# Optimization experiments

Hardware: AMD Instinct MI355X
Metric: run time of the kernel (lower is better)

The kernel has to match this reference:

```python
import jax, jax.numpy as jnp
import numpy as np
from jax import lax

B, D, T = 8, 128, 4096
Q, C = 30, 1024


def setup_inputs() -> dict:
    key = jax.random.key(0)
    k1, k2 = jax.random.split(key)
    x = jax.random.normal(k1, (B, D, T), dtype=jnp.float32)
    codebooks = jax.random.normal(k2, (Q, C, D), dtype=jnp.float32)
    return {"x": x, "codebooks": codebooks}


def _vq_step(residual, cb):
    # residual: [B, T, D], cb: [C, D]
    # argmin over squared euclidean distance; ||r||^2 term is constant per row
    scores = -2.0 * jnp.einsum("btd,cd->btc", residual, cb) + jnp.sum(cb * cb, axis=-1)  # [B,T,C]
    idx = jnp.argmin(scores, axis=-1)          # [B,T]
    quant = cb[idx]                            # [B,T,D] gather
    # commitment loss: mse(quantize.detach(), residual)
    loss = jnp.mean((lax.stop_gradient(quant) - residual) ** 2)
    # straight-through estimator
    quant_st = residual + lax.stop_gradient(quant - residual)
    new_residual = residual - lax.stop_gradient(quant)
    return new_residual, (quant_st, loss)


def reference(x, codebooks):
    # x: [B, D, T] -> [B, T, D]
    xt = jnp.transpose(x, (0, 2, 1))
    _, (quants, losses) = lax.scan(_vq_step, xt, codebooks)  # quants: [Q,B,T,D]
    quantized = jnp.sum(quants, axis=0)                      # [B,T,D]
    quantized = jnp.transpose(quantized, (0, 2, 1))          # [B,D,T]
    commit_loss = jnp.sum(losses)
    return quantized, commit_loss
```

## Files before the change

kernel.cpp:

```cpp
#include <hip/hip_runtime.h>
#include <stdint.h>

#define B_ 8
#define D_ 128
#define T_ 4096
#define Q_ 30
#define C_ 1024

typedef __attribute__((ext_vector_type(8))) short short8;
typedef __attribute__((ext_vector_type(4))) float float4_;

__device__ __align__(16) short g_split[(size_t)Q_*16*16384];

__device__ __forceinline__ unsigned short f2bf(float f){
  unsigned u = __builtin_bit_cast(unsigned, f);
  u += 0x7fffu + ((u>>16)&1u);
  return (unsigned short)(u>>16);
}
__device__ __forceinline__ float bf2f(unsigned short h){
  unsigned u = ((unsigned)h)<<16;
  return __builtin_bit_cast(float, u);
}

typedef __attribute__((address_space(3))) void lds_void;
typedef __attribute__((address_space(1))) const void gbl_void;
__device__ __forceinline__ void gld16(const void* g, void* l){
  __builtin_amdgcn_global_load_lds((gbl_void*)g, (lds_void*)l, 16, 0, 0);
}

__global__ void rvq_prep(const float* __restrict__ cb, float* __restrict__ sumsq){
  int g    = blockIdx.x*128 + (threadIdx.x>>1);
  int half = threadIdx.x & 1;
  const float* src = cb + (size_t)g*D_ + half*64;
  double s = 0.0;
#pragma unroll
  for (int i=0;i<64;i+=4){
    float4_ f = *(const float4_*)(src+i);
    s += (double)f.x*f.x + (double)f.y*f.y + (double)f.z*f.z + (double)f.w*f.w;
  }
  s += __shfl_xor(s, 1);
  if (!half) sumsq[g] = (float)s;
}

__global__ void rvq_split(const float* __restrict__ cb){
  const int bI   = blockIdx.x;
  const int tid  = threadIdx.x;
  const int crel = tid>>2, part = tid&3;
  const int swz  = crel & 15;
  const float* src = cb + ((size_t)(bI*64 + crel))*128 + part*32;
  short* dstH = g_split + ((size_t)bI<<14) + (crel<<7);
#pragma unroll
  for (int i=0;i<32;i+=8){
    float4_ f0 = *(const float4_*)(src+i);
    float4_ f1 = *(const float4_*)(src+i+4);
    float ff[8] = {f0.x,f0.y,f0.z,f0.w,f1.x,f1.y,f1.z,f1.w};
    short8 vh, vl;
#pragma unroll
    for (int j=0;j<8;++j){
      unsigned short hb = f2bf(ff[j]);
      vh[j] = (short)hb;
      vl[j] = (short)f2bf(ff[j] - bf2f(hb));
    }
    const int kgs = ((part<<2) + (i>>3)) ^ swz;
    *(short8*)&dstH[kgs<<3]          = vh;
    *(short8*)&dstH[8192 + (kgs<<3)] = vl;
  }
}

__global__ __launch_bounds__(256,1) void rvq_main(
    const float* __restrict__ x, const float* __restrict__ cb,
    const float* __restrict__ sumsq, double* __restrict__ lossAcc,
    float* __restrict__ out)
{
  __shared__ short sB[2*16384];
  __shared__ float sCcQ[1024];
  __shared__ int   sIdx[2][128];

  const int tid  = threadIdx.x;
  const int wv   = tid>>6;
  const int ln   = tid&63;
  const int col  = ln&15;
  const int quad = ln>>4;
  const int blk  = blockIdx.x;
  const int b    = blk>>5;
  const int t0   = ((blk&31)<<7) + (wv<<5);

  double rmast[2][4][8];
#pragma unroll
  for (int rt=0;rt<2;++rt){
    const int t = t0 + rt*16 + col;
#pragma unroll
    for (int kc=0;kc<4;++kc)
#pragma unroll
      for (int j=0;j<8;++j){
        const int d = kc*32 + quad*8 + j;
        rmast[rt][kc][j] = (double)x[((size_t)b*D_ + d)*T_ + t];
      }
  }

  short8 ah[2][4], al[2][4];
  auto makeAB = [&](){
#pragma unroll
    for (int rt=0;rt<2;++rt)
#pragma unroll
      for (int kc=0;kc<4;++kc){
        short8 h, l;
#pragma unroll
        for (int j=0;j<8;++j){
          float f = (float)rmast[rt][kc][j];
          unsigned short hb = f2bf(f);
          h[j] = (short)hb;
          l[j] = (short)f2bf(f - bf2f(hb));
        }
        ah[rt][kc] = h; al[rt][kc] = l;
      }
  };
  makeAB();

  auto stage = [&](int gqn){
    const char* gsrc = (const char*)g_split + ((size_t)gqn<<15) + (wv<<13) + (ln<<4);
    char* ldst = (char*)sB + ((gqn&1)<<15) + (wv<<13);
#pragma unroll
    for (int it=0; it<8; ++it)
      gld16(gsrc + it*1024, ldst + it*1024);
  };

  for (int i=tid; i<1024; i+=256) sCcQ[i] = sumsq[i];
  stage(0);
  __syncthreads();

  double lossd = 0.0;

  for (int q=0;q<Q_;++q){
    const float* cbq = cb + (size_t)q*C_*D_;

    float m1[2][4], m2[2][4]; int i1[2][4], i2[2][4];
#pragma unroll
    for (int rt=0;rt<2;++rt)
#pragma unroll
      for (int rg=0;rg<4;++rg){
        m1[rt][rg]=3.0e38f; i1[rt][rg]=0;
        m2[rt][rg]=3.0e38f; i2[rt][rg]=0;
      }

    for (int ch=0; ch<16; ++ch){
      const int gq  = q*16 + ch;
      const int nxt = (gq+1 < Q_*16) ? gq+1 : 0;
      stage(nxt);
      asm volatile("s_waitcnt vmcnt(8)" ::: "memory");
      asm volatile("s_barrier" ::: "memory");
      const int bufS = (gq&1)<<14;

#pragma unroll
      for (int itc=0; itc<2; ++itc){
        float4_ acc[2][2];
#pragma unroll
        for (int a=0;a<2;++a)
#pragma unroll
          for (int c=0;c<2;++c) acc[a][c] = (float4_){0.f,0.f,0.f,0.f};
#pragma unroll
        for (int kc=0;kc<4;++kc){
          short8 bh[2], bl[2];
#pragma unroll
          for (int ct=0;ct<2;++ct){
            const int n   = itc*32 + ct*16 + col;
            const int kgs = ((kc<<2) + quad) ^ col;
            bh[ct] = *(const short8*)&sB[bufS + (n<<7) + (kgs<<3)];
            bl[ct] = *(const short8*)&sB[bufS + 8192 + (n<<7) + (kgs<<3)];
          }
#pragma unroll
          for (int rt=0;rt<2;++rt)
#pragma unroll
            for (int ct=0;ct<2;++ct){
              acc[rt][ct] = __builtin_amdgcn_mfma_f32_16x16x32_bf16(ah[rt][kc], bh[ct], acc[rt][ct], 0,0,0);
              acc[rt][ct] = __builtin_amdgcn_mfma_f32_16x16x32_bf16(ah[rt][kc], bl[ct], acc[rt][ct], 0,0,0);
              acc[rt][ct] = __builtin_amdgcn_mfma_f32_16x16x32_bf16(al[rt][kc], bh[ct], acc[rt][ct], 0,0,0);
            }
        }
        const int itg = ch*2 + itc;
#pragma unroll
        for (int ct=0;ct<2;++ct){
          const float cc = sCcQ[(ch<<6) + itc*32 + ct*16 + col];
          const int cid  = itg*2 + ct;
#pragma unroll
          for (int rt=0;rt<2;++rt)
#pragma unroll
            for (int rg=0;rg<4;++rg){
              float s = fmaf(-2.0f, acc[rt][ct][rg], cc);
              if (s < m1[rt][rg]) {
                m2[rt][rg]=m1[rt][rg]; i2[rt][rg]=i1[rt][rg];
                m1[rt][rg]=s;          i1[rt][rg]=cid;
              } else if (s < m2[rt][rg]) {
                m2[rt][rg]=s;          i2[rt][rg]=cid;
              }
            }
        }
      }
      if (ch != 15)
        asm volatile("s_barrier" ::: "memory");
    }

    float a1[2][4], a2[2][4]; int j1[2][4], j2[2][4];
#pragma unroll
    for (int rt=0;rt<2;++rt)
#pragma unroll
      for (int rg=0;rg<4;++rg){
        a1[rt][rg]=m1[rt][rg]; j1[rt][rg]=(i1[rt][rg]<<4)+col;
        a2[rt][rg]=m2[rt][rg]; j2[rt][rg]=(i2[rt][rg]<<4)+col;
      }
#pragma unroll
    for (int mk=1; mk<16; mk<<=1){
#pragma unroll
      for (int rt=0;rt<2;++rt)
#pragma unroll
        for (int rg=0;rg<4;++rg){
          float b1 = __shfl_xor(a1[rt][rg], mk);
          float b2 = __shfl_xor(a2[rt][rg], mk);
          int   k1 = __shfl_xor(j1[rt][rg], mk);
          int   k2 = __shfl_xor(j2[rt][rg], mk);
          float A1=a1[rt][rg], A2=a2[rt][rg]; int J1=j1[rt][rg], J2=j2[rt][rg];
          bool sw  = (b1 < A1) || (b1 == A1 && k1 < J1);
          float w1 = sw ? b1 : A1; int u1 = sw ? k1 : J1;
          float l1 = sw ? A1 : b1; int v1 = sw ? J1 : k1;
          float o2 = sw ? b2 : A2; int ov = sw ? k2 : J2;
          bool t2  = (o2 < l1) || (o2 == l1 && ov < v1);
          a1[rt][rg]=w1; j1[rt][rg]=u1;
          a2[rt][rg]= t2 ? o2 : l1; j2[rt][rg]= t2 ? ov : v1;
        }
    }
    if (col==0){
#pragma unroll
      for (int rt=0;rt<2;++rt)
#pragma unroll
        for (int rg=0;rg<4;++rg){
          const int m = rt*16 + quad*4 + rg;
          sIdx[0][(wv<<5)+m] = j1[rt][rg];
          sIdx[1][(wv<<5)+m] = j2[rt][rg];
        }
    }
    __syncthreads();

#pragma unroll
    for (int rt=0;rt<2;++rt){
      const int m   = rt*16 + col;
      const int jj1 = sIdx[0][(wv<<5)+m];
      const int jj2 = sIdx[1][(wv<<5)+m];
      const float* p1 = cbq + ((size_t)jj1<<7) + (quad<<3);
      const float* p2 = cbq + ((size_t)jj2<<7) + (quad<<3);
      float c1[4][8], c2[4][8];
#pragma unroll
      for (int kc=0;kc<4;++kc){
        float4_ q10 = *(const float4_*)(p1 + kc*32);
        float4_ q11 = *(const float4_*)(p1 + kc*32 + 4);
        float4_ q20 = *(const float4_*)(p2 + kc*32);
        float4_ q21 = *(const float4_*)(p2 + kc*32 + 4);
        c1[kc][0]=q10.x; c1[kc][1]=q10.y; c1[kc][2]=q10.z; c1[kc][3]=q10.w;
        c1[kc][4]=q11.x; c1[kc][5]=q11.y; c1[kc][6]=q11.z; c1[kc][7]=q11.w;
        c2[kc][0]=q20.x; c2[kc][1]=q20.y; c2[kc][2]=q20.z; c2[kc][3]=q20.w;
        c2[kc][4]=q21.x; c2[kc][5]=q21.y; c2[kc][6]=q21.z; c2[kc][7]=q21.w;
      }
      double s1=0.0, s2=0.0;
#pragma unroll
      for (int kc=0;kc<4;++kc)
#pragma unroll
        for (int j=0;j<8;++j){
          double rd  = rmast[rt][kc][j];
          double cd1 = (double)c1[kc][j];
          double cd2 = (double)c2[kc][j];
          s1 += cd1*(cd1 - 2.0*rd);
          s2 += cd2*(cd2 - 2.0*rd);
        }
      s1 += __shfl_xor(s1, 16); s1 += __shfl_xor(s1, 32);
      s2 += __shfl_xor(s2, 16); s2 += __shfl_xor(s2, 32);
      const bool take2 = (s2 < s1) || (s2 == s1 && jj2 < jj1);
#pragma unroll
      for (int kc=0;kc<4;++kc)
#pragma unroll
        for (int j=0;j<8;++j){
          double cw = (double)(take2 ? c2[kc][j] : c1[kc][j]);
          double rn = rmast[rt][kc][j] - cw;
          rmast[rt][kc][j] = rn;
          lossd += rn*rn;
        }
    }
    makeAB();
    if (q+1 < Q_){
      for (int i=tid; i<1024; i+=256) sCcQ[i] = sumsq[(q+1)*1024 + i];
    }
    __syncthreads();
  }

#pragma unroll
  for (int rt=0;rt<2;++rt){
    const int t = t0 + rt*16 + col;
#pragma unroll
    for (int kc=0;kc<4;++kc)
#pragma unroll
      for (int j=0;j<8;++j){
        const int d = kc*32 + quad*8 + j;
        const size_t o = ((size_t)b*D_ + d)*T_ + t;
        out[o] = (float)((double)x[o] - rmast[rt][kc][j]);
      }
  }
#pragma unroll
  for (int mk=1; mk<64; mk<<=1) lossd += __shfl_xor(lossd, mk);
  if (ln==0) atomicAdd(lossAcc, lossd);
}

__global__ void rvq_fin(const double* __restrict__ lossAcc, float* __restrict__ out){
  out[(size_t)B_*D_*T_] = (float)(*lossAcc * (1.0/((double)B_*(double)D_*(double)T_)));
}

extern "C" void kernel_launch(void* const* d_in, const int* in_sizes, int n_in,
                              void* d_out, int out_size, void* d_ws, size_t ws_size,
                              hipStream_t stream) {
  const float* x  = (const float*)d_in[0];
  const float* cb = (const float*)d_in[1];
  float* out      = (float*)d_out;
  double* lossAcc = (double*)d_ws;
  float*  sumsq   = (float*)((char*)d_ws + 256);

  hipMemsetAsync(d_ws, 0, 256, stream);
  rvq_prep <<<Q_*C_/128, 256, 0, stream>>>(cb, sumsq);
  rvq_split<<<Q_*16,     256, 0, stream>>>(cb);
  rvq_main <<<(B_*T_)/128, 256, 0, stream>>>(x, cb, sumsq, lossAcc, out);
  rvq_fin  <<<1, 1, 0, stream>>>(lossAcc, out);
}
```

Baseline: 1.749 ms.

## Split codebook search across two wave halves per row group with LDS merge

Doubles the block to 512 threads: each group of four row-waves is duplicated, and each half scans 512 of the 1024 codewords, staging its own chunk into a doubled LDS buffer. Per-half top-2 candidates go through shared memory and are merged before the exact double-precision rescoring. Only half 0 writes output and loss. This adds waves per CU to hide MFMA and LDS latency, but duplicates the residual registers and rescoring work in both halves and doubles LDS use. The launch bound also changes to 512 threads with 2 blocks per CU.

```diff
diff --git a/kernel.cpp b/kernel.cpp
--- a/kernel.cpp
+++ b/kernel.cpp
@@ -67,23 +67,26 @@
   }
 }
 
-__global__ __launch_bounds__(256,1) void rvq_main(
+__global__ __launch_bounds__(512,2) void rvq_main(
     const float* __restrict__ x, const float* __restrict__ cb,
     const float* __restrict__ sumsq, double* __restrict__ lossAcc,
     float* __restrict__ out)
 {
-  __shared__ short sB[2*16384];
+  __shared__ short sB[2*32768];
   __shared__ float sCcQ[1024];
-  __shared__ int   sIdx[2][128];
+  __shared__ float sMa[4][2][32][2];
+  __shared__ int   sMj[4][2][32][2];
 
   const int tid  = threadIdx.x;
   const int wv   = tid>>6;
   const int ln   = tid&63;
   const int col  = ln&15;
   const int quad = ln>>4;
+  const int hw   = wv>>2;
+  const int rgrp = wv&3;
   const int blk  = blockIdx.x;
   const int b    = blk>>5;
-  const int t0   = ((blk&31)<<7) + (wv<<5);
+  const int t0   = ((blk&31)<<7) + (rgrp<<5);
 
   double rmast[2][4][8];
 #pragma unroll
@@ -117,15 +120,17 @@
   };
   makeAB();
 
-  auto stage = [&](int gqn){
-    const char* gsrc = (const char*)g_split + ((size_t)gqn<<15) + (wv<<13) + (ln<<4);
-    char* ldst = (char*)sB + ((gqn&1)<<15) + (wv<<13);
+  auto stage = [&](int gstep){
+    const int qq = gstep>>3, cc = gstep&7;
+    const int chunk = qq*16 + hw*8 + cc;
+    const char* gsrc = (const char*)g_split + ((size_t)chunk<<15) + (rgrp<<13) + (ln<<4);
+    char* ldst = (char*)sB + ((gstep&1)<<16) + (hw<<15) + (rgrp<<13);
 #pragma unroll
     for (int it=0; it<8; ++it)
       gld16(gsrc + it*1024, ldst + it*1024);
   };
 
-  for (int i=tid; i<1024; i+=256) sCcQ[i] = sumsq[i];
+  for (int i=tid; i<1024; i+=512) sCcQ[i] = sumsq[i];
   stage(0);
   __syncthreads();
 
@@ -143,13 +148,13 @@
         m2[rt][rg]=3.0e38f; i2[rt][rg]=0;
       }
 
-    for (int ch=0; ch<16; ++ch){
-      const int gq  = q*16 + ch;
-      const int nxt = (gq+1 < Q_*16) ? gq+1 : 0;
+    for (int ch=0; ch<8; ++ch){
+      const int gstep = q*8 + ch;
+      const int nxt   = (gstep+1 < Q_*8) ? gstep+1 : 0;
       stage(nxt);
       asm volatile("s_waitcnt vmcnt(8)" ::: "memory");
       asm volatile("s_barrier" ::: "memory");
-      const int bufS = (gq&1)<<14;
+      const int bufS = ((gstep&1)<<15) + (hw<<14);
 
 #pragma unroll
       for (int itc=0; itc<2; ++itc){
@@ -177,11 +182,10 @@
               acc[rt][ct] = __builtin_amdgcn_mfma_f32_16x16x32_bf16(al[rt][kc], bh[ct], acc[rt][ct], 0,0,0);
             }
         }
-        const int itg = ch*2 + itc;
 #pragma unroll
         for (int ct=0;ct<2;++ct){
-          const float cc = sCcQ[(ch<<6) + itc*32 + ct*16 + col];
-          const int cid  = itg*2 + ct;
+          const float cc = sCcQ[(hw<<9) + (ch<<6) + itc*32 + ct*16 + col];
+          const int cid  = ch*4 + itc*2 + ct;
 #pragma unroll
           for (int rt=0;rt<2;++rt)
 #pragma unroll
@@ -196,7 +200,7 @@
             }
         }
       }
-      if (ch != 15)
+      if (ch != 7)
         asm volatile("s_barrier" ::: "memory");
     }
 
@@ -205,8 +209,8 @@
     for (int rt=0;rt<2;++rt)
 #pragma unroll
       for (int rg=0;rg<4;++rg){
-        a1[rt][rg]=m1[rt][rg]; j1[rt][rg]=(i1[rt][rg]<<4)+col;
-        a2[rt][rg]=m2[rt][rg]; j2[rt][rg]=(i2[rt][rg]<<4)+col;
+        a1[rt][rg]=m1[rt][rg]; j1[rt][rg]=(hw<<9)+(i1[rt][rg]<<4)+col;
+        a2[rt][rg]=m2[rt][rg]; j2[rt][rg]=(hw<<9)+(i2[rt][rg]<<4)+col;
       }
 #pragma unroll
     for (int mk=1; mk<16; mk<<=1){
@@ -234,17 +238,27 @@
 #pragma unroll
         for (int rg=0;rg<4;++rg){
           const int m = rt*16 + quad*4 + rg;
-          sIdx[0][(wv<<5)+m] = j1[rt][rg];
-          sIdx[1][(wv<<5)+m] = j2[rt][rg];
+          sMa[rgrp][hw][m][0] = a1[rt][rg];  sMj[rgrp][hw][m][0] = j1[rt][rg];
+          sMa[rgrp][hw][m][1] = a2[rt][rg];  sMj[rgrp][hw][m][1] = j2[rt][rg];
         }
     }
     __syncthreads();
 
 #pragma unroll
     for (int rt=0;rt<2;++rt){
-      const int m   = rt*16 + col;
-      const int jj1 = sIdx[0][(wv<<5)+m];
-      const int jj2 = sIdx[1][(wv<<5)+m];
+      const int m = rt*16 + col;
+      float x1 = sMa[rgrp][0][m][0], x2 = sMa[rgrp][0][m][1];
+      int  xj1 = sMj[rgrp][0][m][0], xj2 = sMj[rgrp][0][m][1];
+      float y1 = sMa[rgrp][1][m][0], y2 = sMa[rgrp][1][m][1];
+      int  yj1 = sMj[rgrp][1][m][0], yj2 = sMj[rgrp][1][m][1];
+      bool sw  = (y1 < x1) || (y1 == x1 && yj1 < xj1);
+      float w1 = sw ? y1 : x1;  int u1 = sw ? yj1 : xj1;
+      float l1 = sw ? x1 : y1;  int v1 = sw ? xj1 : yj1;
+      float o2 = sw ? y2 : x2;  int ov = sw ? yj2 : xj2;
+      bool t2  = (o2 < l1) || (o2 == l1 && ov < v1);
+      const int jj1 = u1;
+      const int jj2 = t2 ? ov : v1;
+
       const float* p1 = cbq + ((size_t)jj1<<7) + (quad<<3);
       const float* p2 = cbq + ((size_t)jj2<<7) + (quad<<3);
       float c1[4][8], c2[4][8];
@@ -285,26 +299,28 @@
     }
     makeAB();
     if (q+1 < Q_){
-      for (int i=tid; i<1024; i+=256) sCcQ[i] = sumsq[(q+1)*1024 + i];
+      for (int i=tid; i<1024; i+=512) sCcQ[i] = sumsq[(q+1)*1024 + i];
     }
     __syncthreads();
   }
 
-#pragma unroll
-  for (int rt=0;rt<2;++rt){
-    const int t = t0 + rt*16 + col;
-#pragma unroll
-    for (int kc=0;kc<4;++kc)
-#pragma unroll
-      for (int j=0;j<8;++j){
-        const int d = kc*32 + quad*8 + j;
-        const size_t o = ((size_t)b*D_ + d)*T_ + t;
-        out[o] = (float)((double)x[o] - rmast[rt][kc][j]);
-      }
-  }
-#pragma unroll
-  for (int mk=1; mk<64; mk<<=1) lossd += __shfl_xor(lossd, mk);
-  if (ln==0) atomicAdd(lossAcc, lossd);
+  if (hw == 0){
+#pragma unroll
+    for (int rt=0;rt<2;++rt){
+      const int t = t0 + rt*16 + col;
+#pragma unroll
+      for (int kc=0;kc<4;++kc)
+#pragma unroll
+        for (int j=0;j<8;++j){
+          const int d = kc*32 + quad*8 + j;
+          const size_t o = ((size_t)b*D_ + d)*T_ + t;
+          out[o] = (float)((double)x[o] - rmast[rt][kc][j]);
+        }
+    }
+#pragma unroll
+    for (int mk=1; mk<64; mk<<=1) lossd += __shfl_xor(lossd, mk);
+    if (ln==0) atomicAdd(lossAcc, lossd);
+  }
 }
 
 __global__ void rvq_fin(const double* __restrict__ lossAcc, float* __restrict__ out){
@@ -323,6 +339,6 @@
   hipMemsetAsync(d_ws, 0, 256, stream);
   rvq_prep <<<Q_*C_/128, 256, 0, stream>>>(cb, sumsq);
   rvq_split<<<Q_*16,     256, 0, stream>>>(cb);
-  rvq_main <<<(B_*T_)/128, 256, 0, stream>>>(x, cb, sumsq, lossAcc, out);
+  rvq_main <<<(B_*T_)/128, 512, 0, stream>>>(x, cb, sumsq, lossAcc, out);
   rvq_fin  <<<1, 1, 0, stream>>>(lossAcc, out);
 }
```

Result: no change. 1.754 ms (+0.3%).

## Split the D reduction across two wave groups per block with LDS partial-sum exchange

Applied to the files above, without the earlier changes.

Doubles the block to 512 threads. Each pair of waves now splits the 128-dim K reduction in half, with the upper half writing partial MFMA accumulators to LDS and the lower half adding them before the argmin. The rescoring and residual update are likewise split, with partial distances exchanged through shared memory. The goal is twice as many waves per CU to hide latency and fewer registers per wave, at the cost of extra LDS traffic and barriers, plus an argmin that only half the waves perform.

```diff
diff --git a/kernel.cpp b/kernel.cpp
--- a/kernel.cpp
+++ b/kernel.cpp
@@ -67,43 +67,47 @@
   }
 }
 
-__global__ __launch_bounds__(256,1) void rvq_main(
+__global__ __launch_bounds__(512,1) void rvq_main(
     const float* __restrict__ x, const float* __restrict__ cb,
     const float* __restrict__ sumsq, double* __restrict__ lossAcc,
     float* __restrict__ out)
 {
-  __shared__ short sB[2*16384];
-  __shared__ float sCcQ[1024];
-  __shared__ int   sIdx[2][128];
+  __shared__ short  sB[2*16384];
+  __shared__ float  sP[8192];
+  __shared__ float  sCcQ[1024];
+  __shared__ int    sIdx[2][128];
+  __shared__ double sS[2][4][2][2][16];
 
   const int tid  = threadIdx.x;
   const int wv   = tid>>6;
   const int ln   = tid&63;
   const int col  = ln&15;
   const int quad = ln>>4;
+  const int dh   = wv>>2;
+  const int rgrp = wv&3;
   const int blk  = blockIdx.x;
   const int b    = blk>>5;
-  const int t0   = ((blk&31)<<7) + (wv<<5);
-
-  double rmast[2][4][8];
+  const int t0   = ((blk&31)<<7) + (rgrp<<5);
+
+  double rmast[2][2][8];
 #pragma unroll
   for (int rt=0;rt<2;++rt){
     const int t = t0 + rt*16 + col;
 #pragma unroll
-    for (int kc=0;kc<4;++kc)
+    for (int kc=0;kc<2;++kc)
 #pragma unroll
       for (int j=0;j<8;++j){
-        const int d = kc*32 + quad*8 + j;
+        const int d = dh*64 + kc*32 + quad*8 + j;
         rmast[rt][kc][j] = (double)x[((size_t)b*D_ + d)*T_ + t];
       }
   }
 
-  short8 ah[2][4], al[2][4];
+  short8 ah[2][2], al[2][2];
   auto makeAB = [&](){
 #pragma unroll
     for (int rt=0;rt<2;++rt)
 #pragma unroll
-      for (int kc=0;kc<4;++kc){
+      for (int kc=0;kc<2;++kc){
         short8 h, l;
 #pragma unroll
         for (int j=0;j<8;++j){
@@ -117,15 +121,15 @@
   };
   makeAB();
 
-  auto stage = [&](int gqn){
-    const char* gsrc = (const char*)g_split + ((size_t)gqn<<15) + (wv<<13) + (ln<<4);
-    char* ldst = (char*)sB + ((gqn&1)<<15) + (wv<<13);
-#pragma unroll
-    for (int it=0; it<8; ++it)
+  auto stage = [&](int c){
+    const char* gsrc = (const char*)g_split + ((size_t)c<<15) + (wv<<12) + (ln<<4);
+    char* ldst = (char*)sB + ((c&1)<<15) + (wv<<12) + (ln<<4);
+#pragma unroll
+    for (int it=0; it<4; ++it)
       gld16(gsrc + it*1024, ldst + it*1024);
   };
 
-  for (int i=tid; i<1024; i+=256) sCcQ[i] = sumsq[i];
+  for (int i=tid; i<1024; i+=512) sCcQ[i] = sumsq[i];
   stage(0);
   __syncthreads();
 
@@ -135,157 +139,191 @@
     const float* cbq = cb + (size_t)q*C_*D_;
 
     float m1[2][4], m2[2][4]; int i1[2][4], i2[2][4];
-#pragma unroll
-    for (int rt=0;rt<2;++rt)
-#pragma unroll
-      for (int rg=0;rg<4;++rg){
-        m1[rt][rg]=3.0e38f; i1[rt][rg]=0;
-        m2[rt][rg]=3.0e38f; i2[rt][rg]=0;
-      }
+    if (dh==0){
+#pragma unroll
+      for (int rt=0;rt<2;++rt)
+#pragma unroll
+        for (int rg=0;rg<4;++rg){
+          m1[rt][rg]=3.0e38f; i1[rt][rg]=0;
+          m2[rt][rg]=3.0e38f; i2[rt][rg]=0;
+        }
+    }
 
     for (int ch=0; ch<16; ++ch){
-      const int gq  = q*16 + ch;
-      const int nxt = (gq+1 < Q_*16) ? gq+1 : 0;
+      const int c   = q*16 + ch;
+      const int nxt = (c+1 < Q_*16) ? c+1 : 0;
       stage(nxt);
-      asm volatile("s_waitcnt vmcnt(8)" ::: "memory");
+      asm volatile("s_waitcnt vmcnt(4)" ::: "memory");
       asm volatile("s_barrier" ::: "memory");
-      const int bufS = (gq&1)<<14;
-
+      const int slot = (c&1)<<14;
+
+      float4_ accT[2][2][2];
 #pragma unroll
       for (int itc=0; itc<2; ++itc){
-        float4_ acc[2][2];
-#pragma unroll
-        for (int a=0;a<2;++a)
-#pragma unroll
-          for (int c=0;c<2;++c) acc[a][c] = (float4_){0.f,0.f,0.f,0.f};
-#pragma unroll
-        for (int kc=0;kc<4;++kc){
+#pragma unroll
+        for (int rt=0;rt<2;++rt)
+#pragma unroll
+          for (int ct=0;ct<2;++ct) accT[itc][rt][ct] = (float4_){0.f,0.f,0.f,0.f};
+#pragma unroll
+        for (int kc=0;kc<2;++kc){
+          const int kgs = ((dh<<3) + (kc<<2) + quad) ^ col;
           short8 bh[2], bl[2];
 #pragma unroll
           for (int ct=0;ct<2;++ct){
-            const int n   = itc*32 + ct*16 + col;
-            const int kgs = ((kc<<2) + quad) ^ col;
-            bh[ct] = *(const short8*)&sB[bufS + (n<<7) + (kgs<<3)];
-            bl[ct] = *(const short8*)&sB[bufS + 8192 + (n<<7) + (kgs<<3)];
+            const int n = itc*32 + ct*16 + col;
+            bh[ct] = *(const short8*)&sB[slot + (n<<7) + (kgs<<3)];
+            bl[ct] = *(const short8*)&sB[slot + 8192 + (n<<7) + (kgs<<3)];
           }
 #pragma unroll
           for (int rt=0;rt<2;++rt)
 #pragma unroll
             for (int ct=0;ct<2;++ct){
-              acc[rt][ct] = __builtin_amdgcn_mfma_f32_16x16x32_bf16(ah[rt][kc], bh[ct], acc[rt][ct], 0,0,0);
-              acc[rt][ct] = __builtin_amdgcn_mfma_f32_16x16x32_bf16(ah[rt][kc], bl[ct], acc[rt][ct], 0,0,0);
-              acc[rt][ct] = __builtin_amdgcn_mfma_f32_16x16x32_bf16(al[rt][kc], bh[ct], acc[rt][ct], 0,0,0);
+              accT[itc][rt][ct] = __builtin_amdgcn_mfma_f32_16x16x32_bf16(ah[rt][kc], bh[ct], accT[itc][rt][ct], 0,0,0);
+              accT[itc][rt][ct] = __builtin_amdgcn_mfma_f32_16x16x32_bf16(ah[rt][kc], bl[ct], accT[itc][rt][ct], 0,0,0);
+              accT[itc][rt][ct] = __builtin_amdgcn_mfma_f32_16x16x32_bf16(al[rt][kc], bh[ct], accT[itc][rt][ct], 0,0,0);
             }
         }
-        const int itg = ch*2 + itc;
-#pragma unroll
-        for (int ct=0;ct<2;++ct){
-          const float cc = sCcQ[(ch<<6) + itc*32 + ct*16 + col];
-          const int cid  = itg*2 + ct;
+        if (dh==1){
 #pragma unroll
           for (int rt=0;rt<2;++rt)
 #pragma unroll
-            for (int rg=0;rg<4;++rg){
-              float s = fmaf(-2.0f, acc[rt][ct][rg], cc);
-              if (s < m1[rt][rg]) {
-                m2[rt][rg]=m1[rt][rg]; i2[rt][rg]=i1[rt][rg];
-                m1[rt][rg]=s;          i1[rt][rg]=cid;
-              } else if (s < m2[rt][rg]) {
-                m2[rt][rg]=s;          i2[rt][rg]=cid;
+            for (int ct=0;ct<2;++ct){
+              const int idx4 = ((((itc*2+rt)*2+ct)*4 + rgrp)*64 + ln)*4;
+              *(float4_*)&sP[idx4] = accT[itc][rt][ct];
+            }
+        }
+      }
+      asm volatile("s_barrier" ::: "memory");
+
+      if (dh==0){
+#pragma unroll
+        for (int itc=0; itc<2; ++itc)
+#pragma unroll
+          for (int ct=0;ct<2;++ct){
+            const float cc = sCcQ[(ch<<6) + itc*32 + ct*16 + col];
+            const int cid  = ch*4 + itc*2 + ct;
+#pragma unroll
+            for (int rt=0;rt<2;++rt){
+              const int idx4 = ((((itc*2+rt)*2+ct)*4 + rgrp)*64 + ln)*4;
+              float4_ p = *(const float4_*)&sP[idx4];
+#pragma unroll
+              for (int rg=0;rg<4;++rg){
+                float tot = accT[itc][rt][ct][rg] + p[rg];
+                float s = fmaf(-2.0f, tot, cc);
+                if (s < m1[rt][rg]) {
+                  m2[rt][rg]=m1[rt][rg]; i2[rt][rg]=i1[rt][rg];
+                  m1[rt][rg]=s;          i1[rt][rg]=cid;
+                } else if (s < m2[rt][rg]) {
+                  m2[rt][rg]=s;          i2[rt][rg]=cid;
+                }
               }
             }
-        }
-      }
-      if (ch != 15)
-        asm volatile("s_barrier" ::: "memory");
-    }
-
-    float a1[2][4], a2[2][4]; int j1[2][4], j2[2][4];
-#pragma unroll
-    for (int rt=0;rt<2;++rt)
-#pragma unroll
-      for (int rg=0;rg<4;++rg){
-        a1[rt][rg]=m1[rt][rg]; j1[rt][rg]=(i1[rt][rg]<<4)+col;
-        a2[rt][rg]=m2[rt][rg]; j2[rt][rg]=(i2[rt][rg]<<4)+col;
-      }
-#pragma unroll
-    for (int mk=1; mk<16; mk<<=1){
+          }
+      }
+    }
+
+    if (dh==0){
+      float a1[2][4], a2[2][4]; int j1[2][4], j2[2][4];
 #pragma unroll
       for (int rt=0;rt<2;++rt)
 #pragma unroll
         for (int rg=0;rg<4;++rg){
-          float b1 = __shfl_xor(a1[rt][rg], mk);
-          float b2 = __shfl_xor(a2[rt][rg], mk);
-          int   k1 = __shfl_xor(j1[rt][rg], mk);
-          int   k2 = __shfl_xor(j2[rt][rg], mk);
-          float A1=a1[rt][rg], A2=a2[rt][rg]; int J1=j1[rt][rg], J2=j2[rt][rg];
-          bool sw  = (b1 < A1) || (b1 == A1 && k1 < J1);
-          float w1 = sw ? b1 : A1; int u1 = sw ? k1 : J1;
-          float l1 = sw ? A1 : b1; int v1 = sw ? J1 : k1;
-          float o2 = sw ? b2 : A2; int ov = sw ? k2 : J2;
-          bool t2  = (o2 < l1) || (o2 == l1 && ov < v1);
-          a1[rt][rg]=w1; j1[rt][rg]=u1;
-          a2[rt][rg]= t2 ? o2 : l1; j2[rt][rg]= t2 ? ov : v1;
-        }
-    }
-    if (col==0){
-#pragma unroll
-      for (int rt=0;rt<2;++rt)
-#pragma unroll
-        for (int rg=0;rg<4;++rg){
-          const int m = rt*16 + quad*4 + rg;
-          sIdx[0][(wv<<5)+m] = j1[rt][rg];
-          sIdx[1][(wv<<5)+m] = j2[rt][rg];
-        }
+          a1[rt][rg]=m1[rt][rg]; j1[rt][rg]=(i1[rt][rg]<<4)+col;
+          a2[rt][rg]=m2[rt][rg]; j2[rt][rg]=(i2[rt][rg]<<4)+col;
+        }
+#pragma unroll
+      for (int mk=1; mk<16; mk<<=1){
+#pragma unroll
+        for (int rt=0;rt<2;++rt)
+#pragma unroll
+          for (int rg=0;rg<4;++rg){
+            float b1 = __shfl_xor(a1[rt][rg], mk);
+            float b2 = __shfl_xor(a2[rt][rg], mk);
+            int   k1 = __shfl_xor(j1[rt][rg], mk);
+            int   k2 = __shfl_xor(j2[rt][rg], mk);
+            float A1=a1[rt][rg], A2=a2[rt][rg]; int J1=j1[rt][rg], J2=j2[rt][rg];
+            bool sw  = (b1 < A1) || (b1 == A1 && k1 < J1);
+            float w1 = sw ? b1 : A1; int u1 = sw ? k1 : J1;
+            float l1 = sw ? A1 : b1; int v1 = sw ? J1 : k1;
+            float o2 = sw ? b2 : A2; int ov = sw ? k2 : J2;
+            bool t2  = (o2 < l1) || (o2 == l1 && ov < v1);
+            a1[rt][rg]=w1; j1[rt][rg]=u1;
+            a2[rt][rg]= t2 ? o2 : l1; j2[rt][rg]= t2 ? ov : v1;
+          }
+      }
+      if (col==0){
+#pragma unroll
+        for (int rt=0;rt<2;++rt)
+#pragma unroll
+          for (int rg=0;rg<4;++rg){
+            const int m = rt*16 + quad*4 + rg;
+            sIdx[0][(rgrp<<5)+m] = j1[rt][rg];
+            sIdx[1][(rgrp<<5)+m] = j2[rt][rg];
+          }
+      }
     }
     __syncthreads();
 
+    int jjA[2][2];
 #pragma unroll
     for (int rt=0;rt<2;++rt){
       const int m   = rt*16 + col;
-      const int jj1 = sIdx[0][(wv<<5)+m];
-      const int jj2 = sIdx[1][(wv<<5)+m];
-      const float* p1 = cbq + ((size_t)jj1<<7) + (quad<<3);
-      const float* p2 = cbq + ((size_t)jj2<<7) + (quad<<3);
-      float c1[4][8], c2[4][8];
-#pragma unroll
-      for (int kc=0;kc<4;++kc){
+      const int jj1 = sIdx[0][(rgrp<<5)+m];
+      const int jj2 = sIdx[1][(rgrp<<5)+m];
+      jjA[rt][0]=jj1; jjA[rt][1]=jj2;
+      const float* p1 = cbq + ((size_t)jj1<<7) + dh*64 + (quad<<3);
+      const float* p2 = cbq + ((size_t)jj2<<7) + dh*64 + (quad<<3);
+      double s1=0.0, s2=0.0;
+#pragma unroll
+      for (int kc=0;kc<2;++kc){
         float4_ q10 = *(const float4_*)(p1 + kc*32);
         float4_ q11 = *(const float4_*)(p1 + kc*32 + 4);
         float4_ q20 = *(const float4_*)(p2 + kc*32);
         float4_ q21 = *(const float4_*)(p2 + kc*32 + 4);
-        c1[kc][0]=q10.x; c1[kc][1]=q10.y; c1[kc][2]=q10.z; c1[kc][3]=q10.w;
-        c1[kc][4]=q11.x; c1[kc][5]=q11.y; c1[kc][6]=q11.z; c1[kc][7]=q11.w;
-        c2[kc][0]=q20.x; c2[kc][1]=q20.y; c2[kc][2]=q20.z; c2[kc][3]=q20.w;
-        c2[kc][4]=q21.x; c2[kc][5]=q21.y; c2[kc][6]=q21.z; c2[kc][7]=q21.w;
-      }
-      double s1=0.0, s2=0.0;
-#pragma unroll
-      for (int kc=0;kc<4;++kc)
+        float f1[8] = {q10.x,q10.y,q10.z,q10.w,q11.x,q11.y,q11.z,q11.w};
+        float f2[8] = {q20.x,q20.y,q20.z,q20.w,q21.x,q21.y,q21.z,q21.w};
 #pragma unroll
         for (int j=0;j<8;++j){
           double rd  = rmast[rt][kc][j];
-          double cd1 = (double)c1[kc][j];
-          double cd2 = (double)c2[kc][j];
+          double cd1 = (double)f1[j];
+          double cd2 = (double)f2[j];
           s1 += cd1*(cd1 - 2.0*rd);
           s2 += cd2*(cd2 - 2.0*rd);
         }
+      }
       s1 += __shfl_xor(s1, 16); s1 += __shfl_xor(s1, 32);
       s2 += __shfl_xor(s2, 16); s2 += __shfl_xor(s2, 32);
-      const bool take2 = (s2 < s1) || (s2 == s1 && jj2 < jj1);
-#pragma unroll
-      for (int kc=0;kc<4;++kc)
+      if (quad==0){
+        sS[dh][rgrp][rt][0][col] = s1;
+        sS[dh][rgrp][rt][1][col] = s2;
+      }
+    }
+    __syncthreads();
+
+#pragma unroll
+    for (int rt=0;rt<2;++rt){
+      const double t1 = sS[0][rgrp][rt][0][col] + sS[1][rgrp][rt][0][col];
+      const double t2 = sS[0][rgrp][rt][1][col] + sS[1][rgrp][rt][1][col];
+      const int jj1 = jjA[rt][0], jj2 = jjA[rt][1];
+      const bool take2 = (t2 < t1) || (t2 == t1 && jj2 < jj1);
+      const int jw = take2 ? jj2 : jj1;
+      const float* pw = cbq + ((size_t)jw<<7) + dh*64 + (quad<<3);
+#pragma unroll
+      for (int kc=0;kc<2;++kc){
+        float4_ w0 = *(const float4_*)(pw + kc*32);
+        float4_ w1 = *(const float4_*)(pw + kc*32 + 4);
+        float fw[8] = {w0.x,w0.y,w0.z,w0.w,w1.x,w1.y,w1.z,w1.w};
 #pragma unroll
         for (int j=0;j<8;++j){
-          double cw = (double)(take2 ? c2[kc][j] : c1[kc][j]);
-          double rn = rmast[rt][kc][j] - cw;
+          double rn = rmast[rt][kc][j] - (double)fw[j];
           rmast[rt][kc][j] = rn;
           lossd += rn*rn;
         }
+      }
     }
     makeAB();
     if (q+1 < Q_){
-      for (int i=tid; i<1024; i+=256) sCcQ[i] = sumsq[(q+1)*1024 + i];
+      for (int i=tid; i<1024; i+=512) sCcQ[i] = sumsq[(q+1)*1024 + i];
     }
     __syncthreads();
   }
@@ -294,10 +332,10 @@
   for (int rt=0;rt<2;++rt){
     const int t = t0 + rt*16 + col;
 #pragma unroll
-    for (int kc=0;kc<4;++kc)
+    for (int kc=0;kc<2;++kc)
 #pragma unroll
       for (int j=0;j<8;++j){
-        const int d = kc*32 + quad*8 + j;
+        const int d = dh*64 + kc*32 + quad*8 + j;
         const size_t o = ((size_t)b*D_ + d)*T_ + t;
         out[o] = (float)((double)x[o] - rmast[rt][kc][j]);
       }
@@ -323,6 +361,6 @@
   hipMemsetAsync(d_ws, 0, 256, stream);
   rvq_prep <<<Q_*C_/128, 256, 0, stream>>>(cb, sumsq);
   rvq_split<<<Q_*16,     256, 0, stream>>>(cb);
-  rvq_main <<<(B_*T_)/128, 256, 0, stream>>>(x, cb, sumsq, lossAcc, out);
+  rvq_main <<<(B_*T_)/128, 512, 0, stream>>>(x, cb, sumsq, lossAcc, out);
   rvq_fin  <<<1, 1, 0, stream>>>(lossAcc, out);
 }
```

Result: no change. 1.730 ms (-1.0%).

## Use single fp16 MFMA pass with top-4 exact fp64 rerank

Applied to the files above, without the earlier changes.

Replaces the three-pass bf16 hi/lo split matmul with one fp16 MFMA per tile and stages fp16 codebook halves, halving staged bytes and cutting MFMA work to a third. To keep argmin exact despite lower precision, per-row candidates are merged into a top-4 list via LDS and rescored in fp64 against the master residual. The risk is that the true nearest code falls outside the candidate set when fp16 errors are large, and extra LDS traffic is added for the candidate reduction.

```diff
diff --git a/kernel.cpp b/kernel.cpp
--- a/kernel.cpp
+++ b/kernel.cpp
@@ -7,20 +7,10 @@
 #define Q_ 30
 #define C_ 1024
 
-typedef __attribute__((ext_vector_type(8))) short short8;
+typedef __attribute__((ext_vector_type(8))) _Float16 half8;
 typedef __attribute__((ext_vector_type(4))) float float4_;
 
-__device__ __align__(16) short g_split[(size_t)Q_*16*16384];
-
-__device__ __forceinline__ unsigned short f2bf(float f){
-  unsigned u = __builtin_bit_cast(unsigned, f);
-  u += 0x7fffu + ((u>>16)&1u);
-  return (unsigned short)(u>>16);
-}
-__device__ __forceinline__ float bf2f(unsigned short h){
-  unsigned u = ((unsigned)h)<<16;
-  return __builtin_bit_cast(float, u);
-}
+__device__ __align__(16) _Float16 g_half[(size_t)Q_*8*16384];
 
 typedef __attribute__((address_space(3))) void lds_void;
 typedef __attribute__((address_space(1))) const void gbl_void;
@@ -45,25 +35,20 @@
 __global__ void rvq_split(const float* __restrict__ cb){
   const int bI   = blockIdx.x;
   const int tid  = threadIdx.x;
-  const int crel = tid>>2, part = tid&3;
+  const int crel = tid>>1, part = tid&1;
   const int swz  = crel & 15;
-  const float* src = cb + ((size_t)(bI*64 + crel))*128 + part*32;
-  short* dstH = g_split + ((size_t)bI<<14) + (crel<<7);
-#pragma unroll
-  for (int i=0;i<32;i+=8){
-    float4_ f0 = *(const float4_*)(src+i);
-    float4_ f1 = *(const float4_*)(src+i+4);
-    float ff[8] = {f0.x,f0.y,f0.z,f0.w,f1.x,f1.y,f1.z,f1.w};
-    short8 vh, vl;
-#pragma unroll
-    for (int j=0;j<8;++j){
-      unsigned short hb = f2bf(ff[j]);
-      vh[j] = (short)hb;
-      vl[j] = (short)f2bf(ff[j] - bf2f(hb));
-    }
-    const int kgs = ((part<<2) + (i>>3)) ^ swz;
-    *(short8*)&dstH[kgs<<3]          = vh;
-    *(short8*)&dstH[8192 + (kgs<<3)] = vl;
+  const float* src = cb + ((size_t)bI*128 + crel)*128 + part*64;
+  _Float16* dst = g_half + ((size_t)bI<<14) + (crel<<7);
+#pragma unroll
+  for (int i=0;i<8;++i){
+    float4_ f0 = *(const float4_*)(src + i*8);
+    float4_ f1 = *(const float4_*)(src + i*8 + 4);
+    half8 h;
+    h[0]=(_Float16)f0.x; h[1]=(_Float16)f0.y; h[2]=(_Float16)f0.z; h[3]=(_Float16)f0.w;
+    h[4]=(_Float16)f1.x; h[5]=(_Float16)f1.y; h[6]=(_Float16)f1.z; h[7]=(_Float16)f1.w;
+    const int kg  = part*8 + i;
+    const int kgs = kg ^ swz;
+    *(half8*)&dst[kgs<<3] = h;
   }
 }
 
@@ -72,9 +57,11 @@
     const float* __restrict__ sumsq, double* __restrict__ lossAcc,
     float* __restrict__ out)
 {
-  __shared__ short sB[2*16384];
+  __shared__ _Float16 sBh[2*16384];
+  __shared__ float sCS[4][32][16][2];
+  __shared__ int   sCI[4][32][16][2];
+  __shared__ int   sI4[4][32][4];
   __shared__ float sCcQ[1024];
-  __shared__ int   sIdx[2][128];
 
   const int tid  = threadIdx.x;
   const int wv   = tid>>6;
@@ -98,28 +85,23 @@
       }
   }
 
-  short8 ah[2][4], al[2][4];
+  half8 ah[2][4];
   auto makeAB = [&](){
 #pragma unroll
     for (int rt=0;rt<2;++rt)
 #pragma unroll
       for (int kc=0;kc<4;++kc){
-        short8 h, l;
-#pragma unroll
-        for (int j=0;j<8;++j){
-          float f = (float)rmast[rt][kc][j];
-          unsigned short hb = f2bf(f);
-          h[j] = (short)hb;
-          l[j] = (short)f2bf(f - bf2f(hb));
-        }
-        ah[rt][kc] = h; al[rt][kc] = l;
+        half8 h;
+#pragma unroll
+        for (int j=0;j<8;++j) h[j] = (_Float16)(float)rmast[rt][kc][j];
+        ah[rt][kc] = h;
       }
   };
   makeAB();
 
-  auto stage = [&](int gqn){
-    const char* gsrc = (const char*)g_split + ((size_t)gqn<<15) + (wv<<13) + (ln<<4);
-    char* ldst = (char*)sB + ((gqn&1)<<15) + (wv<<13);
+  auto stage = [&](int c){
+    const char* gsrc = (const char*)g_half + ((size_t)c<<15) + (wv<<13) + (ln<<4);
+    char* ldst = (char*)sBh + ((c&1)<<15) + (wv<<13) + (ln<<4);
 #pragma unroll
     for (int it=0; it<8; ++it)
       gld16(gsrc + it*1024, ldst + it*1024);
@@ -143,45 +125,40 @@
         m2[rt][rg]=3.0e38f; i2[rt][rg]=0;
       }
 
-    for (int ch=0; ch<16; ++ch){
-      const int gq  = q*16 + ch;
-      const int nxt = (gq+1 < Q_*16) ? gq+1 : 0;
+    for (int ch=0; ch<8; ++ch){
+      const int gstep = q*8 + ch;
+      const int nxt   = (gstep+1 < Q_*8) ? gstep+1 : 0;
       stage(nxt);
       asm volatile("s_waitcnt vmcnt(8)" ::: "memory");
       asm volatile("s_barrier" ::: "memory");
-      const int bufS = (gq&1)<<14;
-
-#pragma unroll
-      for (int itc=0; itc<2; ++itc){
+      const int slot = (gstep&1)<<14;
+
+#pragma unroll
+      for (int itc=0; itc<4; ++itc){
         float4_ acc[2][2];
 #pragma unroll
         for (int a=0;a<2;++a)
 #pragma unroll
-          for (int c=0;c<2;++c) acc[a][c] = (float4_){0.f,0.f,0.f,0.f};
+          for (int c2=0;c2<2;++c2) acc[a][c2] = (float4_){0.f,0.f,0.f,0.f};
 #pragma unroll
         for (int kc=0;kc<4;++kc){
-          short8 bh[2], bl[2];
+          const int kgs = ((kc<<2) + quad) ^ col;
+          half8 bf[2];
 #pragma unroll
           for (int ct=0;ct<2;++ct){
-            const int n   = itc*32 + ct*16 + col;
-            const int kgs = ((kc<<2) + quad) ^ col;
-            bh[ct] = *(const short8*)&sB[bufS + (n<<7) + (kgs<<3)];
-            bl[ct] = *(const short8*)&sB[bufS + 8192 + (n<<7) + (kgs<<3)];
+            const int n = itc*32 + ct*16 + col;
+            bf[ct] = *(const half8*)&sBh[slot + (n<<7) + (kgs<<3)];
           }
 #pragma unroll
           for (int rt=0;rt<2;++rt)
 #pragma unroll
-            for (int ct=0;ct<2;++ct){
-              acc[rt][ct] = __builtin_amdgcn_mfma_f32_16x16x32_bf16(ah[rt][kc], bh[ct], acc[rt][ct], 0,0,0);
-              acc[rt][ct] = __builtin_amdgcn_mfma_f32_16x16x32_bf16(ah[rt][kc], bl[ct], acc[rt][ct], 0,0,0);
-              acc[rt][ct] = __builtin_amdgcn_mfma_f32_16x16x32_bf16(al[rt][kc], bh[ct], acc[rt][ct], 0,0,0);
-            }
-        }
-        const int itg = ch*2 + itc;
+            for (int ct=0;ct<2;++ct)
+              acc[rt][ct] = __builtin_amdgcn_mfma_f32_16x16x32_f16(ah[rt][kc], bf[ct], acc[rt][ct], 0,0,0);
+        }
 #pragma unroll
         for (int ct=0;ct<2;++ct){
-          const float cc = sCcQ[(ch<<6) + itc*32 + ct*16 + col];
-          const int cid  = itg*2 + ct;
+          const float cc = sCcQ[(ch<<7) + itc*32 + ct*16 + col];
+          const int cid  = ch*8 + itc*2 + ct;
 #pragma unroll
           for (int rt=0;rt<2;++rt)
 #pragma unroll
@@ -196,92 +173,81 @@
             }
         }
       }
-      if (ch != 15)
+      if (ch != 7)
         asm volatile("s_barrier" ::: "memory");
     }
 
-    float a1[2][4], a2[2][4]; int j1[2][4], j2[2][4];
 #pragma unroll
     for (int rt=0;rt<2;++rt)
 #pragma unroll
       for (int rg=0;rg<4;++rg){
-        a1[rt][rg]=m1[rt][rg]; j1[rt][rg]=(i1[rt][rg]<<4)+col;
-        a2[rt][rg]=m2[rt][rg]; j2[rt][rg]=(i2[rt][rg]<<4)+col;
-      }
-#pragma unroll
-    for (int mk=1; mk<16; mk<<=1){
-#pragma unroll
-      for (int rt=0;rt<2;++rt)
-#pragma unroll
-        for (int rg=0;rg<4;++rg){
-          float b1 = __shfl_xor(a1[rt][rg], mk);
-          float b2 = __shfl_xor(a2[rt][rg], mk);
-          int   k1 = __shfl_xor(j1[rt][rg], mk);
-          int   k2 = __shfl_xor(j2[rt][rg], mk);
-          float A1=a1[rt][rg], A2=a2[rt][rg]; int J1=j1[rt][rg], J2=j2[rt][rg];
-          bool sw  = (b1 < A1) || (b1 == A1 && k1 < J1);
-          float w1 = sw ? b1 : A1; int u1 = sw ? k1 : J1;
-          float l1 = sw ? A1 : b1; int v1 = sw ? J1 : k1;
-          float o2 = sw ? b2 : A2; int ov = sw ? k2 : J2;
-          bool t2  = (o2 < l1) || (o2 == l1 && ov < v1);
-          a1[rt][rg]=w1; j1[rt][rg]=u1;
-          a2[rt][rg]= t2 ? o2 : l1; j2[rt][rg]= t2 ? ov : v1;
-        }
-    }
-    if (col==0){
-#pragma unroll
-      for (int rt=0;rt<2;++rt)
-#pragma unroll
-        for (int rg=0;rg<4;++rg){
-          const int m = rt*16 + quad*4 + rg;
-          sIdx[0][(wv<<5)+m] = j1[rt][rg];
-          sIdx[1][(wv<<5)+m] = j2[rt][rg];
-        }
-    }
-    __syncthreads();
+        const int row = rt*16 + quad*4 + rg;
+        sCS[wv][row][col][0] = m1[rt][rg];  sCI[wv][row][col][0] = (i1[rt][rg]<<4)+col;
+        sCS[wv][row][col][1] = m2[rt][rg];  sCI[wv][row][col][1] = (i2[rt][rg]<<4)+col;
+      }
+
+    if (ln < 32){
+      const int row = ln;
+      float b0=3.0e38f,b1=3.0e38f,b2=3.0e38f,b3=3.0e38f;
+      int   e0=0x7fffffff,e1=0x7fffffff,e2=0x7fffffff,e3=0x7fffffff;
+#pragma unroll
+      for (int c2=0;c2<32;++c2){
+        const float s = sCS[wv][row][c2>>1][c2&1];
+        const int  id = sCI[wv][row][c2>>1][c2&1];
+        const bool l0 = (s<b0)||(s==b0&&id<e0);
+        const bool l1 = (s<b1)||(s==b1&&id<e1);
+        const bool l2 = (s<b2)||(s==b2&&id<e2);
+        const bool l3 = (s<b3)||(s==b3&&id<e3);
+        if (l3){
+          b3 = l2 ? b2 : s;  e3 = l2 ? e2 : id;
+          if (l2){
+            b2 = l1 ? b1 : s;  e2 = l1 ? e1 : id;
+            if (l1){
+              b1 = l0 ? b0 : s;  e1 = l0 ? e0 : id;
+              if (l0){ b0 = s; e0 = id; }
+            }
+          }
+        }
+      }
+      sI4[wv][row][0]=e0; sI4[wv][row][1]=e1; sI4[wv][row][2]=e2; sI4[wv][row][3]=e3;
+    }
 
 #pragma unroll
     for (int rt=0;rt<2;++rt){
-      const int m   = rt*16 + col;
-      const int jj1 = sIdx[0][(wv<<5)+m];
-      const int jj2 = sIdx[1][(wv<<5)+m];
-      const float* p1 = cbq + ((size_t)jj1<<7) + (quad<<3);
-      const float* p2 = cbq + ((size_t)jj2<<7) + (quad<<3);
-      float c1[4][8], c2[4][8];
+      const int m = rt*16 + col;
+      double bestS = 1.0e300; int bestJ = 0x7fffffff;
+#pragma unroll
+      for (int cnd=0;cnd<4;++cnd){
+        const int jj = sI4[wv][m][cnd];
+        const float* p = cbq + ((size_t)jj<<7) + (quad<<3);
+        double s = 0.0;
+#pragma unroll
+        for (int kc=0;kc<4;++kc){
+          float4_ a0 = *(const float4_*)(p + kc*32);
+          float4_ a1 = *(const float4_*)(p + kc*32 + 4);
+          float fv[8] = {a0.x,a0.y,a0.z,a0.w,a1.x,a1.y,a1.z,a1.w};
+#pragma unroll
+          for (int j=0;j<8;++j){
+            double cd = (double)fv[j];
+            s += cd*(cd - 2.0*rmast[rt][kc][j]);
+          }
+        }
+        s += __shfl_xor(s, 16); s += __shfl_xor(s, 32);
+        if ((s < bestS) || (s == bestS && jj < bestJ)){ bestS = s; bestJ = jj; }
+      }
+      const float* pw = cbq + ((size_t)bestJ<<7) + (quad<<3);
 #pragma unroll
       for (int kc=0;kc<4;++kc){
-        float4_ q10 = *(const float4_*)(p1 + kc*32);
-        float4_ q11 = *(const float4_*)(p1 + kc*32 + 4);
-        float4_ q20 = *(const float4_*)(p2 + kc*32);
-        float4_ q21 = *(const float4_*)(p2 + kc*32 + 4);
-        c1[kc][0]=q10.x; c1[kc][1]=q10.y; c1[kc][2]=q10.z; c1[kc][3]=q10.w;
-        c1[kc][4]=q11.x; c1[kc][5]=q11.y; c1[kc][6]=q11.z; c1[kc][7]=q11.w;
-        c2[kc][0]=q20.x; c2[kc][1]=q20.y; c2[kc][2]=q20.z; c2[kc][3]=q20.w;
-        c2[kc][4]=q21.x; c2[kc][5]=q21.y; c2[kc][6]=q21.z; c2[kc][7]=q21.w;
-      }
-      double s1=0.0, s2=0.0;
-#pragma unroll
-      for (int kc=0;kc<4;++kc)
+        float4_ w0 = *(const float4_*)(pw + kc*32);
+        float4_ w1 = *(const float4_*)(pw + kc*32 + 4);
+        float fw[8] = {w0.x,w0.y,w0.z,w0.w,w1.x,w1.y,w1.z,w1.w};
 #pragma unroll
         for (int j=0;j<8;++j){
-          double rd  = rmast[rt][kc][j];
-          double cd1 = (double)c1[kc][j];
-          double cd2 = (double)c2[kc][j];
-          s1 += cd1*(cd1 - 2.0*rd);
-          s2 += cd2*(cd2 - 2.0*rd);
-        }
-      s1 += __shfl_xor(s1, 16); s1 += __shfl_xor(s1, 32);
-      s2 += __shfl_xor(s2, 16); s2 += __shfl_xor(s2, 32);
-      const bool take2 = (s2 < s1) || (s2 == s1 && jj2 < jj1);
-#pragma unroll
-      for (int kc=0;kc<4;++kc)
-#pragma unroll
-        for (int j=0;j<8;++j){
-          double cw = (double)(take2 ? c2[kc][j] : c1[kc][j]);
-          double rn = rmast[rt][kc][j] - cw;
+          double rn = rmast[rt][kc][j] - (double)fw[j];
           rmast[rt][kc][j] = rn;
           lossd += rn*rn;
         }
+      }
     }
     makeAB();
     if (q+1 < Q_){
@@ -322,7 +288,7 @@
 
   hipMemsetAsync(d_ws, 0, 256, stream);
   rvq_prep <<<Q_*C_/128, 256, 0, stream>>>(cb, sumsq);
-  rvq_split<<<Q_*16,     256, 0, stream>>>(cb);
+  rvq_split<<<Q_*8,      256, 0, stream>>>(cb);
   rvq_main <<<(B_*T_)/128, 256, 0, stream>>>(x, cb, sumsq, lossAcc, out);
   rvq_fin  <<<1, 1, 0, stream>>>(lossAcc, out);
 }
```

Result: slower. 1.944 ms (+11.2%).
